# Kernel optimization log

Measured on AMD Instinct MI355X. Metric: run time of the kernel, lower is better.

Reference implementation:

```python
import jax, jax.numpy as jnp
import numpy as np

MAX_AGENTS = 64
IN_DIM = 256
HID_DIM = 512
OUT_DIM = 256
MAX_CHILDREN = 8
BATCH = 1024


def setup_inputs() -> dict:
    key = jax.random.key(0)
    k1, k2, k3, k4, k5 = jax.random.split(key, 5)
    W1 = jax.random.normal(k1, (MAX_AGENTS, IN_DIM, HID_DIM), dtype=jnp.float32) * 0.02
    b1 = jnp.zeros((MAX_AGENTS, HID_DIM), dtype=jnp.float32)
    W2 = jax.random.normal(k2, (MAX_AGENTS, HID_DIM, OUT_DIM), dtype=jnp.float32) * 0.02
    b2 = jnp.zeros((MAX_AGENTS, OUT_DIM), dtype=jnp.float32)
    router_weights = jax.random.normal(k3, (MAX_AGENTS, HID_DIM, MAX_CHILDREN), dtype=jnp.float32) * 0.01
    agent_indices = jax.random.randint(k4, (BATCH,), 0, MAX_AGENTS, dtype=jnp.int64 if jax.config.jax_enable_x64 else jnp.int32)
    x = jax.random.normal(k5, (BATCH, IN_DIM), dtype=jnp.float32)
    return {
        "x": x,
        "W1": W1,
        "b1": b1,
        "W2": W2,
        "b2": b2,
        "router_weights": router_weights,
        "agent_indices": agent_indices,
    }


def reference(x, W1, b1, W2, b2, router_weights, agent_indices):
    # Gather per-sample weights (same as torch advanced indexing W1[agent_indices])
    w1 = W1[agent_indices]           # [B, In, Hid]
    b1g = b1[agent_indices]          # [B, Hid]
    w2 = W2[agent_indices]           # [B, Hid, Out]
    b2g = b2[agent_indices]          # [B, Out]
    rw = router_weights[agent_indices]  # [B, Hid, C]

    # per-sample MLP: bmm with a singleton row -> einsum
    h = jax.nn.relu(jnp.einsum('bi,bih->bh', x, w1) + b1g)      # [B, Hid]
    out = jnp.einsum('bh,bho->bo', h, w2) + b2g                 # [B, Out]
    r_logits = jnp.einsum('bh,bhc->bc', h, rw)                  # [B, C]
    return (h, out, r_logits)
```

## Files before the change

### kernel.cpp

```cpp
#include <hip/hip_runtime.h>

#define IN_DIM   256
#define HID_DIM  512
#define OUT_DIM  256
#define N_CHILD  8
#define BATCH    1024

#define SB    16
#define XPAD  20
#define MAXCH 128

extern "C" __global__ __launch_bounds__(1024)
void prep_sort(const int* __restrict__ raw, int* __restrict__ sorted,
               int* __restrict__ ch_agent, int* __restrict__ ch_start,
               int* __restrict__ ch_len)
{
    __shared__ int cnt[64], start[64];
    __shared__ int is32;
    const int t = threadIdx.x;
    if (t < 64) cnt[t] = 0;
    if (t == 0) is32 = 0;
    __syncthreads();
    if (raw[2 * (t & 511) + 1] != 0) is32 = 1;
    __syncthreads();
    const int a = (is32 ? raw[t] : raw[2 * t]) & 63;
    atomicAdd(&cnt[a], 1);
    __syncthreads();
    if (t == 0) {
        int off = 0, nch = 0;
        for (int i = 0; i < 64; ++i) {
            start[i] = off;
            const int c = cnt[i];
            for (int p = 0; p < c; p += SB) {
                ch_agent[nch] = i;
                ch_start[nch] = off + p;
                ch_len[nch]   = (c - p < SB) ? (c - p) : SB;
                ++nch;
            }
            off += c;
        }
        for (; nch < MAXCH; ++nch) ch_len[nch] = 0;
    }
    __syncthreads();
    if (t < 64) cnt[t] = 0;
    __syncthreads();
    const int pos = start[a] + atomicAdd(&cnt[a], 1);
    sorted[pos] = t;
}

extern "C" __global__ __launch_bounds__(256)
void k1_mlp1(const float* __restrict__ x, const float* __restrict__ W1,
             const float* __restrict__ b1, const float* __restrict__ rw,
             const int* __restrict__ sorted, const int* __restrict__ ch_agent,
             const int* __restrict__ ch_start, const int* __restrict__ ch_len,
             float* __restrict__ h_out, float* __restrict__ r_out)
{
    const int chunk = blockIdx.x;
    const int len = ch_len[chunk];
    if (len == 0) return;
    const int a  = ch_agent[chunk];
    const int cs = ch_start[chunk];
    const int t  = threadIdx.x;
    const int bcol = blockIdx.y * 64;

    __shared__ float xT[IN_DIM * XPAD];
    __shared__ float wS[2][64 * 64];
    __shared__ int   sid[SB];

    if (t < SB) sid[t] = sorted[cs + (t < len ? t : len - 1)];
    __syncthreads();

    #pragma unroll
    for (int s = 0; s < SB; ++s)
        xT[t * XPAD + s] = x[(size_t)sid[s] * IN_DIM + t];

    const float* Wb = W1 + (size_t)a * IN_DIM * HID_DIM + bcol;
    #pragma unroll
    for (int i = 0; i < 4; ++i) {
        const int id  = t + i * 256;
        const int row = id >> 4;
        const int c4  = (id & 15) * 4;
        *(float4*)(&wS[0][row * 64 + c4]) =
            *(const float4*)(Wb + (size_t)row * HID_DIM + c4);
    }
    __syncthreads();

    const int cg = t & 15;
    const int kq = (t >> 4) & 3;
    const int w  = t >> 6;
    const bool act = (w * 4) < len;

    float acc[16];
    #pragma unroll
    for (int i = 0; i < 16; ++i) acc[i] = 0.f;

    for (int p = 0; p < IN_DIM / 64; ++p) {
        if (p < 3) {
            const int nb = (p + 1) & 1;
            const float* Wp = Wb + (size_t)(p + 1) * 64 * HID_DIM;
            #pragma unroll
            for (int i = 0; i < 4; ++i) {
                const int id  = t + i * 256;
                const int row = id >> 4;
                const int c4  = (id & 15) * 4;
                *(float4*)(&wS[nb][row * 64 + c4]) =
                    *(const float4*)(Wp + (size_t)row * HID_DIM + c4);
            }
        }
        if (act) {
            const float* wb = wS[p & 1];
            #pragma unroll
            for (int i = 0; i < 16; ++i) {
                const int row = kq * 16 + i;
                const float4 wv = *(const float4*)(&wb[row * 64 + cg * 4]);
                const float4 xv = *(const float4*)(&xT[(p * 64 + row) * XPAD + w * 4]);
                const float wa[4] = {wv.x, wv.y, wv.z, wv.w};
                const float xa[4] = {xv.x, xv.y, xv.z, xv.w};
                #pragma unroll
                for (int c = 0; c < 4; ++c)
                    #pragma unroll
                    for (int s = 0; s < 4; ++s)
                        acc[c * 4 + s] = fmaf(wa[c], xa[s], acc[c * 4 + s]);
            }
        }
        __syncthreads();
    }

    if (!act) return;

    #pragma unroll
    for (int i = 0; i < 16; ++i) {
        acc[i] += __shfl_xor(acc[i], 16);
        acc[i] += __shfl_xor(acc[i], 32);
    }

    const float4 bv = *(const float4*)(b1 + a * HID_DIM + bcol + cg * 4);
    const float ba[4] = {bv.x, bv.y, bv.z, bv.w};
    float hv[16];
    #pragma unroll
    for (int c = 0; c < 4; ++c)
        #pragma unroll
        for (int s = 0; s < 4; ++s)
            hv[c * 4 + s] = fmaxf(acc[c * 4 + s] + ba[c], 0.f);

    if (kq == 0) {
        #pragma unroll
        for (int s = 0; s < 4; ++s) {
            float4 v = make_float4(hv[0 * 4 + s], hv[1 * 4 + s],
                                   hv[2 * 4 + s], hv[3 * 4 + s]);
            *(float4*)(h_out + (size_t)sid[w * 4 + s] * HID_DIM + bcol + cg * 4) = v;
        }
    }

    float rp[32];
    #pragma unroll
    for (int i = 0; i < 32; ++i) rp[i] = 0.f;
    const float* rwa = rw + (size_t)a * HID_DIM * N_CHILD + (size_t)(bcol + cg * 4) * N_CHILD;
    #pragma unroll
    for (int j = 0; j < 4; ++j)
        #pragma unroll
        for (int ch = 0; ch < 8; ++ch) {
            const float rv = rwa[j * N_CHILD + ch];
            #pragma unroll
            for (int s = 0; s < 4; ++s)
                rp[s * 8 + ch] = fmaf(hv[j * 4 + s], rv, rp[s * 8 + ch]);
        }
    #pragma unroll
    for (int i = 0; i < 32; ++i) {
        rp[i] += __shfl_xor(rp[i], 1);
        rp[i] += __shfl_xor(rp[i], 2);
        rp[i] += __shfl_xor(rp[i], 4);
        rp[i] += __shfl_xor(rp[i], 8);
    }
    if (cg == 0 && kq == 0) {
        #pragma unroll
        for (int s = 0; s < 4; ++s) {
            const int sg = w * 4 + s;
            if (sg < len) {
                float* rdst = r_out + (size_t)sid[sg] * N_CHILD;
                #pragma unroll
                for (int ch = 0; ch < 8; ++ch)
                    atomicAdd(rdst + ch, rp[s * 8 + ch]);
            }
        }
    }
}

extern "C" __global__ __launch_bounds__(256)
void k2_mlp2(const float* __restrict__ h, const float* __restrict__ W2,
             const float* __restrict__ b2,
             const int* __restrict__ sorted, const int* __restrict__ ch_agent,
             const int* __restrict__ ch_start, const int* __restrict__ ch_len,
             float* __restrict__ o_out)
{
    const int chunk = blockIdx.x;
    const int len = ch_len[chunk];
    if (len == 0) return;
    const int a  = ch_agent[chunk];
    const int cs = ch_start[chunk];
    const int t  = threadIdx.x;
    const int bcol = blockIdx.y * 64;

    __shared__ float hT[2][64 * XPAD];
    __shared__ float wS[2][64 * 64];
    __shared__ int   sid[SB];

    if (t < SB) sid[t] = sorted[cs + (t < len ? t : len - 1)];
    __syncthreads();

    const float* Wb = W2 + (size_t)a * HID_DIM * OUT_DIM + bcol;
    {
        const int row = t & 63;
        const int sb  = (t >> 6) * 4;
        #pragma unroll
        for (int j = 0; j < 4; ++j)
            hT[0][row * XPAD + sb + j] = h[(size_t)sid[sb + j] * HID_DIM + row];
        #pragma unroll
        for (int i = 0; i < 4; ++i) {
            const int id  = t + i * 256;
            const int r2  = id >> 4;
            const int c4  = (id & 15) * 4;
            *(float4*)(&wS[0][r2 * 64 + c4]) =
                *(const float4*)(Wb + (size_t)r2 * OUT_DIM + c4);
        }
    }
    __syncthreads();

    const int cg = t & 15;
    const int kq = (t >> 4) & 3;
    const int w  = t >> 6;
    const bool act = (w * 4) < len;

    float acc[16];
    #pragma unroll
    for (int i = 0; i < 16; ++i) acc[i] = 0.f;

    for (int p = 0; p < HID_DIM / 64; ++p) {
        if (p < 7) {
            const int nb = (p + 1) & 1;
            const int k0 = (p + 1) * 64;
            const int row = t & 63;
            const int sb  = (t >> 6) * 4;
            #pragma unroll
            for (int j = 0; j < 4; ++j)
                hT[nb][row * XPAD + sb + j] =
                    h[(size_t)sid[sb + j] * HID_DIM + k0 + row];
            const float* Wp = Wb + (size_t)k0 * OUT_DIM;
            #pragma unroll
            for (int i = 0; i < 4; ++i) {
                const int id  = t + i * 256;
                const int r2  = id >> 4;
                const int c4  = (id & 15) * 4;
                *(float4*)(&wS[nb][r2 * 64 + c4]) =
                    *(const float4*)(Wp + (size_t)r2 * OUT_DIM + c4);
            }
        }
        if (act) {
            const float* wb = wS[p & 1];
            const float* hb = hT[p & 1];
            #pragma unroll
            for (int i = 0; i < 16; ++i) {
                const int row = kq * 16 + i;
                const float4 wv = *(const float4*)(&wb[row * 64 + cg * 4]);
                const float4 xv = *(const float4*)(&hb[row * XPAD + w * 4]);
                const float wa[4] = {wv.x, wv.y, wv.z, wv.w};
                const float xa[4] = {xv.x, xv.y, xv.z, xv.w};
                #pragma unroll
                for (int c = 0; c < 4; ++c)
                    #pragma unroll
                    for (int s = 0; s < 4; ++s)
                        acc[c * 4 + s] = fmaf(wa[c], xa[s], acc[c * 4 + s]);
            }
        }
        __syncthreads();
    }

    if (!act) return;
    #pragma unroll
    for (int i = 0; i < 16; ++i) {
        acc[i] += __shfl_xor(acc[i], 16);
        acc[i] += __shfl_xor(acc[i], 32);
    }
    if (kq == 0) {
        const float4 bv = *(const float4*)(b2 + a * OUT_DIM + bcol + cg * 4);
        #pragma unroll
        for (int s = 0; s < 4; ++s) {
            float4 v = make_float4(acc[0 * 4 + s] + bv.x, acc[1 * 4 + s] + bv.y,
                                   acc[2 * 4 + s] + bv.z, acc[3 * 4 + s] + bv.w);
            *(float4*)(o_out + (size_t)sid[w * 4 + s] * OUT_DIM + bcol + cg * 4) = v;
        }
    }
}

extern "C" void kernel_launch(void* const* d_in, const int* in_sizes, int n_in,
                              void* d_out, int out_size, void* d_ws, size_t ws_size,
                              hipStream_t stream) {
    const float* x  = (const float*)d_in[0];
    const float* W1 = (const float*)d_in[1];
    const float* b1 = (const float*)d_in[2];
    const float* W2 = (const float*)d_in[3];
    const float* b2 = (const float*)d_in[4];
    const float* rw = (const float*)d_in[5];
    const int* raw  = (const int*)d_in[6];

    int* ws       = (int*)d_ws;
    int* sorted   = ws;
    int* ch_agent = ws + 1024;
    int* ch_start = ws + 1152;
    int* ch_len   = ws + 1280;

    float* out   = (float*)d_out;
    float* h_out = out;
    float* o_out = h_out + (size_t)BATCH * HID_DIM;
    float* r_out = o_out + (size_t)BATCH * OUT_DIM;

    hipMemsetAsync(r_out, 0, (size_t)BATCH * N_CHILD * sizeof(float), stream);
    hipLaunchKernelGGL(prep_sort, dim3(1), dim3(1024), 0, stream,
                       raw, sorted, ch_agent, ch_start, ch_len);
    hipLaunchKernelGGL(k1_mlp1, dim3(MAXCH, 8), dim3(256), 0, stream,
                       x, W1, b1, rw, sorted, ch_agent, ch_start, ch_len,
                       h_out, r_out);
    hipLaunchKernelGGL(k2_mlp2, dim3(MAXCH, 4), dim3(256), 0, stream,
                       h_out, W2, b2, sorted, ch_agent, ch_start, ch_len, o_out);
}
```

Before: 144.1 us.

## Split-K the second MLP kernel with atomics and parallelize chunk-table prefix scan

The second GEMM kernel now splits the hidden (K) dimension in two along a new grid z-axis. Each half accumulates into the output with float atomicAdd, bias is added only by the z=0 half, and the output region is zeroed with the memset up front. This doubles the block count to better fill the GPU, at the cost of atomic traffic and a larger memset. Separately, the serial single-thread chunk-table build in prep_sort is replaced by a 64-lane wavefront prefix scan over per-agent counts.

```diff
diff --git a/kernel.cpp b/kernel.cpp
--- a/kernel.cpp
+++ b/kernel.cpp
@@ -15,10 +15,10 @@
                int* __restrict__ ch_agent, int* __restrict__ ch_start,
                int* __restrict__ ch_len)
 {
-    __shared__ int cnt[64], start[64];
-    __shared__ int is32;
+    __shared__ int cnt[64], cnt2[64], start[64];
+    __shared__ int is32, totch;
     const int t = threadIdx.x;
-    if (t < 64) cnt[t] = 0;
+    if (t < 64) { cnt[t] = 0; cnt2[t] = 0; }
     if (t == 0) is32 = 0;
     __syncthreads();
     if (raw[2 * (t & 511) + 1] != 0) is32 = 1;
@@ -26,25 +26,29 @@
     const int a = (is32 ? raw[t] : raw[2 * t]) & 63;
     atomicAdd(&cnt[a], 1);
     __syncthreads();
-    if (t == 0) {
-        int off = 0, nch = 0;
-        for (int i = 0; i < 64; ++i) {
-            start[i] = off;
-            const int c = cnt[i];
-            for (int p = 0; p < c; p += SB) {
-                ch_agent[nch] = i;
-                ch_start[nch] = off + p;
-                ch_len[nch]   = (c - p < SB) ? (c - p) : SB;
-                ++nch;
-            }
-            off += c;
-        }
-        for (; nch < MAXCH; ++nch) ch_len[nch] = 0;
-    }
-    __syncthreads();
-    if (t < 64) cnt[t] = 0;
-    __syncthreads();
-    const int pos = start[a] + atomicAdd(&cnt[a], 1);
+    if (t < 64) {
+        const int c   = cnt[t];
+        const int nch = (c + SB - 1) / SB;
+        int sc = c, sn = nch;
+        #pragma unroll
+        for (int d = 1; d < 64; d <<= 1) {
+            const int vc = __shfl_up(sc, d);
+            const int vn = __shfl_up(sn, d);
+            if (t >= d) { sc += vc; sn += vn; }
+        }
+        const int off = sc - c;
+        start[t] = off;
+        const int chb = sn - nch;
+        for (int p = 0, j = 0; p < c; p += SB, ++j) {
+            ch_agent[chb + j] = t;
+            ch_start[chb + j] = off + p;
+            ch_len[chb + j]   = (c - p < SB) ? (c - p) : SB;
+        }
+        if (t == 63) totch = sn;
+    }
+    __syncthreads();
+    if (t >= totch && t < MAXCH) ch_len[t] = 0;
+    const int pos = start[a] + atomicAdd(&cnt2[a], 1);
     sorted[pos] = t;
 }
 
@@ -200,6 +204,7 @@
     const int cs = ch_start[chunk];
     const int t  = threadIdx.x;
     const int bcol = blockIdx.y * 64;
+    const int kb   = blockIdx.z * 256;
 
     __shared__ float hT[2][64 * XPAD];
     __shared__ float wS[2][64 * 64];
@@ -214,14 +219,15 @@
         const int sb  = (t >> 6) * 4;
         #pragma unroll
         for (int j = 0; j < 4; ++j)
-            hT[0][row * XPAD + sb + j] = h[(size_t)sid[sb + j] * HID_DIM + row];
+            hT[0][row * XPAD + sb + j] =
+                h[(size_t)sid[sb + j] * HID_DIM + kb + row];
         #pragma unroll
         for (int i = 0; i < 4; ++i) {
             const int id  = t + i * 256;
             const int r2  = id >> 4;
             const int c4  = (id & 15) * 4;
             *(float4*)(&wS[0][r2 * 64 + c4]) =
-                *(const float4*)(Wb + (size_t)r2 * OUT_DIM + c4);
+                *(const float4*)(Wb + (size_t)(kb + r2) * OUT_DIM + c4);
         }
     }
     __syncthreads();
@@ -235,10 +241,10 @@
     #pragma unroll
     for (int i = 0; i < 16; ++i) acc[i] = 0.f;
 
-    for (int p = 0; p < HID_DIM / 64; ++p) {
-        if (p < 7) {
+    for (int p = 0; p < 4; ++p) {
+        if (p < 3) {
             const int nb = (p + 1) & 1;
-            const int k0 = (p + 1) * 64;
+            const int k0 = kb + (p + 1) * 64;
             const int row = t & 63;
             const int sb  = (t >> 6) * 4;
             #pragma unroll
@@ -282,12 +288,19 @@
         acc[i] += __shfl_xor(acc[i], 32);
     }
     if (kq == 0) {
-        const float4 bv = *(const float4*)(b2 + a * OUT_DIM + bcol + cg * 4);
+        float4 bv = make_float4(0.f, 0.f, 0.f, 0.f);
+        if (blockIdx.z == 0)
+            bv = *(const float4*)(b2 + a * OUT_DIM + bcol + cg * 4);
         #pragma unroll
         for (int s = 0; s < 4; ++s) {
-            float4 v = make_float4(acc[0 * 4 + s] + bv.x, acc[1 * 4 + s] + bv.y,
-                                   acc[2 * 4 + s] + bv.z, acc[3 * 4 + s] + bv.w);
-            *(float4*)(o_out + (size_t)sid[w * 4 + s] * OUT_DIM + bcol + cg * 4) = v;
+            const int g = w * 4 + s;
+            if (g < len) {
+                float* op = o_out + (size_t)sid[g] * OUT_DIM + bcol + cg * 4;
+                atomicAdd(op + 0, acc[0 * 4 + s] + bv.x);
+                atomicAdd(op + 1, acc[1 * 4 + s] + bv.y);
+                atomicAdd(op + 2, acc[2 * 4 + s] + bv.z);
+                atomicAdd(op + 3, acc[3 * 4 + s] + bv.w);
+            }
         }
     }
 }
@@ -314,12 +327,13 @@
     float* o_out = h_out + (size_t)BATCH * HID_DIM;
     float* r_out = o_out + (size_t)BATCH * OUT_DIM;
 
-    hipMemsetAsync(r_out, 0, (size_t)BATCH * N_CHILD * sizeof(float), stream);
+    hipMemsetAsync(o_out, 0,
+                   (size_t)BATCH * (OUT_DIM + N_CHILD) * sizeof(float), stream);
     hipLaunchKernelGGL(prep_sort, dim3(1), dim3(1024), 0, stream,
                        raw, sorted, ch_agent, ch_start, ch_len);
     hipLaunchKernelGGL(k1_mlp1, dim3(MAXCH, 8), dim3(256), 0, stream,
                        x, W1, b1, rw, sorted, ch_agent, ch_start, ch_len,
                        h_out, r_out);
-    hipLaunchKernelGGL(k2_mlp2, dim3(MAXCH, 4), dim3(256), 0, stream,
+    hipLaunchKernelGGL(k2_mlp2, dim3(MAXCH, 4, 2), dim3(256), 0, stream,
                        h_out, W2, b2, sorted, ch_agent, ch_start, ch_len, o_out);
 }
```

New measurement: 134.1 us. 6.9% less time.
